# Kernel optimization log

Hardware: AMD Instinct MI355X
Metric: run time of the kernel (lower is better)

Reference implementation:

```python
import jax, jax.numpy as jnp
import numpy as np

T, B, E, H = 1024, 4, 1024, 16
D = E // H  # head_dim = 64


def rel_shift(x):
    # Transformer-XL relative shift trick (RelativeShift.forward, batch_first=True).
    # x: [BH, Q, P] -> pad one zero column, reshape [BH, P+1, Q], drop first row, reshape back.
    BH, Q, P = x.shape
    zp = jnp.zeros((BH, Q, 1), x.dtype)
    xp = jnp.concatenate([zp, x], axis=2).reshape(BH, P + 1, Q)
    return xp[:, 1:, :].reshape(BH, Q, P)


def setup_inputs() -> dict:
    key = jax.random.key(0)
    ks = jax.random.split(key, 8)
    std = float(np.sqrt(2.0 / (E + E)))
    causal = jnp.triu(jnp.ones((T, T), dtype=bool), k=1)  # True = masked (future positions)
    return {
        "x": jax.random.normal(ks[0], (T, B, E), dtype=jnp.float32),
        "pos": jax.random.normal(ks[1], (T, 1, E), dtype=jnp.float32),
        "in_proj_weight": jax.random.normal(ks[2], (3 * E, E), dtype=jnp.float32) * std,
        "in_proj_bias": jnp.zeros((3 * E,), dtype=jnp.float32),
        "out_proj_weight": jax.random.normal(ks[3], (E, E), dtype=jnp.float32) * std,
        "out_proj_bias": jnp.zeros((E,), dtype=jnp.float32),
        "pos_proj_weight": jax.random.normal(ks[4], (E, E), dtype=jnp.float32) * std,
        "pos_proj_bias": jnp.zeros((E,), dtype=jnp.float32),
        "r_w_bias": jax.random.normal(ks[5], (H, D), dtype=jnp.float32) * 0.02,
        "r_r_bias": jax.random.normal(ks[6], (H, D), dtype=jnp.float32) * 0.02,
        "attn_mask": causal,
    }


def reference(x, pos, in_proj_weight, in_proj_bias, out_proj_weight, out_proj_bias,
              pos_proj_weight, pos_proj_bias, r_w_bias, r_r_bias, attn_mask):
    Tq, Bb, Ee = x.shape
    scale = 1.0 / np.sqrt(D).astype(np.float32)
    # fused QKV projection; layout [T, B, heads, 3, head_dim] matches
    # view(len_q, bsz*heads, 3, head_dim) in the original.
    qkv = (x @ in_proj_weight.T + in_proj_bias).reshape(Tq, Bb, H, 3, D)
    q = qkv[..., 0, :]  # [T,B,H,D]
    k = qkv[..., 1, :]
    v = qkv[..., 2, :]
    # position projection (shared across batch since pos is [T,1,E])
    r_head_k = (pos[:, 0, :] @ pos_proj_weight.T + pos_proj_bias).reshape(Tq, H, D)  # [P,H,D]
    rw_q = q + r_w_bias  # content bias
    rr_q = q + r_r_bias  # position bias
    ac = jnp.einsum('qbhd,kbhd->bhqk', rw_q, k) * scale            # [B,H,Q,K]
    bd = jnp.einsum('qbhd,phd->bhqp', rr_q, r_head_k) * scale      # [B,H,Q,P]
    bd = rel_shift(bd.reshape(Bb * H, Tq, Tq)).reshape(Bb, H, Tq, Tq)[..., :Tq]
    score = ac + bd
    score = jnp.where(attn_mask[None, None, :, :], -jnp.inf, score)
    attn = jax.nn.softmax(score, axis=-1)                          # [B,H,Q,K]
    ctx = jnp.einsum('bhqk,kbhd->qbhd', attn, v).reshape(Tq, Bb, Ee)
    out = ctx @ out_proj_weight.T + out_proj_bias                  # [T,B,E]
    return out, attn
```

## Files before the change

### kernel.cpp

```cpp
#include <hip/hip_runtime.h>
#include <math.h>

#define TQ 1024
#define BBATCH 4
#define EDIM 1024
#define HHEADS 16
#define DHEAD 64

typedef __bf16 bf16x8 __attribute__((ext_vector_type(8)));
typedef __bf16 bf16x4 __attribute__((ext_vector_type(4)));
typedef float  f32x4  __attribute__((ext_vector_type(4)));

#define LDK 40

template<int MODE>
__global__ __launch_bounds__(256) void gemm_mfma_abt(
    const float* __restrict__ A, const float* __restrict__ B,
    const float* __restrict__ bias, float* __restrict__ C,
    int M, int N, int K)
{
    __shared__ __bf16 As[128 * LDK];
    __shared__ __bf16 Bs[128 * LDK];
    const int tid  = threadIdx.x;
    const int lane = tid & 63;
    const int wid  = tid >> 6;
    const int wr   = wid >> 1, wc = wid & 1;
    const int m0 = blockIdx.y * 128, n0 = blockIdx.x * 128;

    f32x4 acc[4][4] = {};

    const int sm0 = tid >> 2;
    const int sm1 = sm0 + 64;
    const int sk  = (tid & 3) << 3;

    const int fr = lane & 15;
    const int kg = (lane >> 4) << 3;

    for (int k0 = 0; k0 < K; k0 += 32) {
        float4 ra0a = *(const float4*)&A[(size_t)(m0 + sm0) * K + k0 + sk];
        float4 ra0b = *(const float4*)&A[(size_t)(m0 + sm0) * K + k0 + sk + 4];
        float4 ra1a = *(const float4*)&A[(size_t)(m0 + sm1) * K + k0 + sk];
        float4 ra1b = *(const float4*)&A[(size_t)(m0 + sm1) * K + k0 + sk + 4];
        float4 rb0a = *(const float4*)&B[(size_t)(n0 + sm0) * K + k0 + sk];
        float4 rb0b = *(const float4*)&B[(size_t)(n0 + sm0) * K + k0 + sk + 4];
        float4 rb1a = *(const float4*)&B[(size_t)(n0 + sm1) * K + k0 + sk];
        float4 rb1b = *(const float4*)&B[(size_t)(n0 + sm1) * K + k0 + sk + 4];

        __syncthreads();

        bf16x8 w;
        w[0]=(__bf16)ra0a.x; w[1]=(__bf16)ra0a.y; w[2]=(__bf16)ra0a.z; w[3]=(__bf16)ra0a.w;
        w[4]=(__bf16)ra0b.x; w[5]=(__bf16)ra0b.y; w[6]=(__bf16)ra0b.z; w[7]=(__bf16)ra0b.w;
        *(bf16x8*)&As[sm0 * LDK + sk] = w;
        w[0]=(__bf16)ra1a.x; w[1]=(__bf16)ra1a.y; w[2]=(__bf16)ra1a.z; w[3]=(__bf16)ra1a.w;
        w[4]=(__bf16)ra1b.x; w[5]=(__bf16)ra1b.y; w[6]=(__bf16)ra1b.z; w[7]=(__bf16)ra1b.w;
        *(bf16x8*)&As[sm1 * LDK + sk] = w;
        w[0]=(__bf16)rb0a.x; w[1]=(__bf16)rb0a.y; w[2]=(__bf16)rb0a.z; w[3]=(__bf16)rb0a.w;
        w[4]=(__bf16)rb0b.x; w[5]=(__bf16)rb0b.y; w[6]=(__bf16)rb0b.z; w[7]=(__bf16)rb0b.w;
        *(bf16x8*)&Bs[sm0 * LDK + sk] = w;
        w[0]=(__bf16)rb1a.x; w[1]=(__bf16)rb1a.y; w[2]=(__bf16)rb1a.z; w[3]=(__bf16)rb1a.w;
        w[4]=(__bf16)rb1b.x; w[5]=(__bf16)rb1b.y; w[6]=(__bf16)rb1b.z; w[7]=(__bf16)rb1b.w;
        *(bf16x8*)&Bs[sm1 * LDK + sk] = w;

        __syncthreads();

        bf16x8 af[4], bfr[4];
        #pragma unroll
        for (int i = 0; i < 4; ++i) {
            af[i]  = *(const bf16x8*)&As[(wr * 64 + i * 16 + fr) * LDK + kg];
            bfr[i] = *(const bf16x8*)&Bs[(wc * 64 + i * 16 + fr) * LDK + kg];
        }
        #pragma unroll
        for (int mi = 0; mi < 4; ++mi)
        #pragma unroll
        for (int ni = 0; ni < 4; ++ni)
            acc[mi][ni] = __builtin_amdgcn_mfma_f32_16x16x32_bf16(
                af[mi], bfr[ni], acc[mi][ni], 0, 0, 0);
    }

    const int fq = lane >> 4;
    #pragma unroll
    for (int mi = 0; mi < 4; ++mi)
    #pragma unroll
    for (int ni = 0; ni < 4; ++ni) {
        int row = m0 + wr * 64 + mi * 16 + fq * 4;
        int col = n0 + wc * 64 + ni * 16 + fr;
        float bv = bias[col];
        #pragma unroll
        for (int j = 0; j < 4; ++j) {
            float v = acc[mi][ni][j] + bv;
            if (MODE == 0) {
                C[(size_t)(row + j) * N + col] = v;
            } else {
                C[(((size_t)(col >> 6) << 10) + (row + j)) * 64 + (col & 63)] = v;
            }
        }
    }
}

__global__ __launch_bounds__(256) void bias_dots_kernel(
    const float* __restrict__ qkv, const float* __restrict__ Rm,
    const float* __restrict__ rwb, const float* __restrict__ rrb,
    float* __restrict__ cK, float* __restrict__ cR)
{
    int id = blockIdx.x * 256 + threadIdx.x;
    if (id < 65536) {
        int bh = id >> 10, k = id & 1023;
        int b = bh >> 4, h = bh & 15;
        const float* p = &qkv[((size_t)k * 4 + b) * 3072 + h * 192 + 64];
        const float* w = &rwb[h << 6];
        float s = 0.f;
        #pragma unroll
        for (int d = 0; d < 64; d += 4) {
            float4 v = *(const float4*)&p[d];
            s += v.x * w[d] + v.y * w[d + 1] + v.z * w[d + 2] + v.w * w[d + 3];
        }
        cK[id] = s;
    } else if (id < 81920) {
        int id2 = id - 65536;
        int h = id2 >> 10, j = id2 & 1023;
        const float* p = &Rm[(((size_t)h << 10) + j) * 64];
        const float* w = &rrb[h << 6];
        float s = 0.f;
        #pragma unroll
        for (int d = 0; d < 64; d += 4) {
            float4 v = *(const float4*)&p[d];
            s += v.x * w[d] + v.y * w[d + 1] + v.z * w[d + 2] + v.w * w[d + 3];
        }
        cR[id2] = s;
    }
}

#define SLD 72

__global__ __launch_bounds__(256) void score_mfma_kernel(
    const float* __restrict__ qkv, const float* __restrict__ Rm,
    const float* __restrict__ cK, const float* __restrict__ cR,
    float* __restrict__ attn)
{
    int t = blockIdx.x;
    int qt = (int)((sqrtf(8.f * t + 1.f) - 1.f) * 0.5f);
    while ((qt + 1) * (qt + 2) / 2 <= t) ++qt;
    while (qt * (qt + 1) / 2 > t) --qt;
    int kt = t - qt * (qt + 1) / 2;

    const int bh = blockIdx.y;
    const int b = bh >> 4, h = bh & 15;
    const int q0 = qt << 6, k0 = kt << 6;
    const int tid = threadIdx.x, lane = tid & 63, wid = tid >> 6;
    const int fr = lane & 15, fq = lane >> 4, kg = fq << 3;
    const int w16 = wid << 4;
    const int base_j = k0 - q0 + 960;

    __shared__ __bf16 Qs[64 * SLD];
    __shared__ __bf16 Ks[64 * SLD];
    __shared__ __bf16 Rs[64 * SLD];
    __shared__ float  BDs[64][68];

    float4 qreg[4], kreg[4], r0reg[4], r1reg[4];
    #pragma unroll
    for (int s = 0; s < 4; ++s) {
        int idx = (s << 8) + tid;
        int r = idx >> 4, dc = (idx & 15) << 2;
        qreg[s] = *(const float4*)&qkv[((size_t)(q0 + r) * 4 + b) * 3072 + h * 192 + dc];
        kreg[s] = *(const float4*)&qkv[((size_t)(k0 + r) * 4 + b) * 3072 + h * 192 + 64 + dc];
        int j0 = base_j + r;       if (j0 > 1023) j0 = 1023;
        int j1 = base_j + 64 + r;  if (j1 > 1023) j1 = 1023;
        r0reg[s] = *(const float4*)&Rm[(((size_t)h << 10) + j0) * 64 + dc];
        r1reg[s] = *(const float4*)&Rm[(((size_t)h << 10) + j1) * 64 + dc];
    }
    #pragma unroll
    for (int s = 0; s < 4; ++s) {
        int idx = (s << 8) + tid;
        int r = idx >> 4, dc = (idx & 15) << 2;
        bf16x4 w;
        w[0]=(__bf16)qreg[s].x; w[1]=(__bf16)qreg[s].y; w[2]=(__bf16)qreg[s].z; w[3]=(__bf16)qreg[s].w;
        *(bf16x4*)&Qs[r * SLD + dc] = w;
        w[0]=(__bf16)kreg[s].x; w[1]=(__bf16)kreg[s].y; w[2]=(__bf16)kreg[s].z; w[3]=(__bf16)kreg[s].w;
        *(bf16x4*)&Ks[r * SLD + dc] = w;
        w[0]=(__bf16)r0reg[s].x; w[1]=(__bf16)r0reg[s].y; w[2]=(__bf16)r0reg[s].z; w[3]=(__bf16)r0reg[s].w;
        *(bf16x4*)&Rs[r * SLD + dc] = w;
    }
    __syncthreads();

    bf16x8 af0 = *(const bf16x8*)&Qs[(w16 + fr) * SLD + kg];
    bf16x8 af1 = *(const bf16x8*)&Qs[(w16 + fr) * SLD + 32 + kg];

    f32x4 aac[4], abd[4];
    const f32x4 zero4 = {0.f, 0.f, 0.f, 0.f};

    #pragma unroll
    for (int ni = 0; ni < 4; ++ni) {
        bf16x8 b0 = *(const bf16x8*)&Ks[(ni * 16 + fr) * SLD + kg];
        bf16x8 b1 = *(const bf16x8*)&Ks[(ni * 16 + fr) * SLD + 32 + kg];
        aac[ni] = __builtin_amdgcn_mfma_f32_16x16x32_bf16(af0, b0, zero4, 0, 0, 0);
        aac[ni] = __builtin_amdgcn_mfma_f32_16x16x32_bf16(af1, b1, aac[ni], 0, 0, 0);
    }
    #pragma unroll
    for (int ni = 0; ni < 4; ++ni) {
        bf16x8 b0 = *(const bf16x8*)&Rs[(ni * 16 + fr) * SLD + kg];
        bf16x8 b1 = *(const bf16x8*)&Rs[(ni * 16 + fr) * SLD + 32 + kg];
        abd[ni] = __builtin_amdgcn_mfma_f32_16x16x32_bf16(af0, b0, zero4, 0, 0, 0);
        abd[ni] = __builtin_amdgcn_mfma_f32_16x16x32_bf16(af1, b1, abd[ni], 0, 0, 0);
    }
    #pragma unroll
    for (int ni = 0; ni < 4; ++ni)
    #pragma unroll
    for (int j = 0; j < 4; ++j)
        BDs[w16 + fq * 4 + j][ni * 16 + fr] = abd[ni][j];
    asm volatile("s_waitcnt lgkmcnt(0)" ::: "memory");
    #pragma unroll
    for (int ni = 0; ni < 4; ++ni)
    #pragma unroll
    for (int j = 0; j < 4; ++j) {
        int lrow = w16 + fq * 4 + j;
        int widx = (ni * 16 + fr) - lrow + 63;
        if (widx < 64) aac[ni][j] += BDs[lrow][widx];
    }
    __syncthreads();

    #pragma unroll
    for (int s = 0; s < 4; ++s) {
        int idx = (s << 8) + tid;
        int r = idx >> 4, dc = (idx & 15) << 2;
        bf16x4 w;
        w[0]=(__bf16)r1reg[s].x; w[1]=(__bf16)r1reg[s].y; w[2]=(__bf16)r1reg[s].z; w[3]=(__bf16)r1reg[s].w;
        *(bf16x4*)&Rs[r * SLD + dc] = w;
    }
    __syncthreads();

    #pragma unroll
    for (int ni = 0; ni < 4; ++ni) {
        bf16x8 b0 = *(const bf16x8*)&Rs[(ni * 16 + fr) * SLD + kg];
        bf16x8 b1 = *(const bf16x8*)&Rs[(ni * 16 + fr) * SLD + 32 + kg];
        abd[ni] = __builtin_amdgcn_mfma_f32_16x16x32_bf16(af0, b0, zero4, 0, 0, 0);
        abd[ni] = __builtin_amdgcn_mfma_f32_16x16x32_bf16(af1, b1, abd[ni], 0, 0, 0);
    }
    #pragma unroll
    for (int ni = 0; ni < 4; ++ni)
    #pragma unroll
    for (int j = 0; j < 4; ++j)
        BDs[w16 + fq * 4 + j][ni * 16 + fr] = abd[ni][j];
    asm volatile("s_waitcnt lgkmcnt(0)" ::: "memory");
    #pragma unroll
    for (int ni = 0; ni < 4; ++ni)
    #pragma unroll
    for (int j = 0; j < 4; ++j) {
        int lrow = w16 + fq * 4 + j;
        int widx = (ni * 16 + fr) - lrow + 63;
        if (widx >= 64) aac[ni][j] += BDs[lrow][widx - 64];
    }

    #pragma unroll
    for (int ni = 0; ni < 4; ++ni) {
        int lcol = ni * 16 + fr;
        int k = k0 + lcol;
        float ckv = cK[(bh << 10) + k];
        #pragma unroll
        for (int j = 0; j < 4; ++j) {
            int lrow = w16 + fq * 4 + j;
            int q = q0 + lrow;
            int widx = lcol - lrow + 63;
            int jidx = base_j + widx; if (jidx > 1023) jidx = 1023;
            float crv = cR[(h << 10) + jidx];
            float v = 0.125f * (aac[ni][j] + ckv + crv);
            if (kt == qt && lcol > lrow) v = -1e30f;
            attn[((((size_t)bh << 10) + q) << 10) + k] = v;
        }
    }
}

__global__ __launch_bounds__(256) void row_stats_kernel(
    const float* __restrict__ attn, float2* __restrict__ stats)
{
    const int gw = blockIdx.x * 4 + (threadIdx.x >> 6);
    const int bh = gw >> 10, q = gw & 1023;
    const int lane = threadIdx.x & 63;
    const float* row = attn + ((size_t)bh << 20) + ((size_t)q << 10);

    float m = -1e30f, s = 0.f;
    const int nc = (q >> 8) + 1;
    for (int c = 0; c < nc; ++c) {
        int base = (c << 8) + (lane << 2);
        float4 v = *(const float4*)&row[base];
        bool c0 = base + 0 <= q, c1 = base + 1 <= q, c2 = base + 2 <= q, c3 = base + 3 <= q;
        float e0 = c0 ? v.x : -1e30f, e1 = c1 ? v.y : -1e30f;
        float e2 = c2 ? v.z : -1e30f, e3 = c3 ? v.w : -1e30f;
        float tm = fmaxf(fmaxf(e0, e1), fmaxf(e2, e3));
        float mn = fmaxf(m, tm);
        s *= __expf(m - mn);
        if (c0) s += __expf(v.x - mn);
        if (c1) s += __expf(v.y - mn);
        if (c2) s += __expf(v.z - mn);
        if (c3) s += __expf(v.w - mn);
        m = mn;
    }
    #pragma unroll
    for (int off = 1; off < 64; off <<= 1) {
        float mo = __shfl_xor(m, off), so = __shfl_xor(s, off);
        float mn = fmaxf(m, mo);
        s = s * __expf(m - mn) + so * __expf(mo - mn);
        m = mn;
    }
    if (lane == 0) stats[gw] = make_float2(m, 1.0f / s);
}

#define FLD 66

__global__ __launch_bounds__(256) void ctx_norm_kernel(
    const float* __restrict__ qkv, const float2* __restrict__ stats,
    float* __restrict__ attn, float* __restrict__ ctx)
{
    const int qt = 15 - blockIdx.x;
    const int bh = blockIdx.y;
    const int b = bh >> 4, h = bh & 15;
    const int q0 = qt << 6;
    const int tid = threadIdx.x, lane = tid & 63, wid = tid >> 6;
    const int fr = lane & 15, fq = lane >> 4, kg = fq << 3;
    const int w16 = wid << 4;

    __shared__ __bf16 Pl[64 * FLD];
    __shared__ __bf16 Vt[64 * FLD];

    float mrow[4], inv[4];
    #pragma unroll
    for (int j = 0; j < 4; ++j) {
        float2 st = stats[(bh << 10) + q0 + w16 + fq * 4 + j];
        mrow[j] = st.x; inv[j] = st.y;
    }

    f32x4 apv[4] = {};
    for (int kt = 0; kt <= qt; ++kt) {
        const int k0 = kt << 6;
        float4 vreg[4];
        #pragma unroll
        for (int s = 0; s < 4; ++s) {
            int idx = (s << 8) + tid, r = idx >> 4, dc = (idx & 15) << 2;
            vreg[s] = *(const float4*)&qkv[((size_t)(k0 + r) * 4 + b) * 3072 + h * 192 + 128 + dc];
        }
        float praw[4][4];
        #pragma unroll
        for (int ni = 0; ni < 4; ++ni)
        #pragma unroll
        for (int j = 0; j < 4; ++j)
            praw[ni][j] = attn[((size_t)bh << 20) +
                               ((size_t)(q0 + w16 + fq * 4 + j) << 10) + k0 + ni * 16 + fr];
        __syncthreads();
        #pragma unroll
        for (int s = 0; s < 4; ++s) {
            int idx = (s << 8) + tid, r = idx >> 4, dc = (idx & 15) << 2;
            Vt[(dc + 0) * FLD + r] = (__bf16)vreg[s].x;
            Vt[(dc + 1) * FLD + r] = (__bf16)vreg[s].y;
            Vt[(dc + 2) * FLD + r] = (__bf16)vreg[s].z;
            Vt[(dc + 3) * FLD + r] = (__bf16)vreg[s].w;
        }
        #pragma unroll
        for (int ni = 0; ni < 4; ++ni)
        #pragma unroll
        for (int j = 0; j < 4; ++j) {
            float p = __expf(praw[ni][j] - mrow[j]) * inv[j];
            attn[((size_t)bh << 20) +
                 ((size_t)(q0 + w16 + fq * 4 + j) << 10) + k0 + ni * 16 + fr] = p;
            Pl[(w16 + fq * 4 + j) * FLD + ni * 16 + fr] = (__bf16)p;
        }
        __syncthreads();
        bf16x8 pa0 = *(const bf16x8*)&Pl[(w16 + fr) * FLD + kg];
        bf16x8 pa1 = *(const bf16x8*)&Pl[(w16 + fr) * FLD + 32 + kg];
        #pragma unroll
        for (int ni = 0; ni < 4; ++ni) {
            bf16x8 bv0 = *(const bf16x8*)&Vt[(ni * 16 + fr) * FLD + kg];
            bf16x8 bv1 = *(const bf16x8*)&Vt[(ni * 16 + fr) * FLD + 32 + kg];
            apv[ni] = __builtin_amdgcn_mfma_f32_16x16x32_bf16(pa0, bv0, apv[ni], 0, 0, 0);
            apv[ni] = __builtin_amdgcn_mfma_f32_16x16x32_bf16(pa1, bv1, apv[ni], 0, 0, 0);
        }
    }

    for (int kt = qt + 1; kt < 16; ++kt) {
        const int k0 = kt << 6;
        #pragma unroll
        for (int s = 0; s < 4; ++s) {
            int idx = (s << 8) + tid, r = idx >> 4, c4 = (idx & 15) << 2;
            float4 z = {0.f, 0.f, 0.f, 0.f};
            *(float4*)&attn[((size_t)bh << 20) + ((size_t)(q0 + r) << 10) + k0 + c4] = z;
        }
    }
    #pragma unroll
    for (int ni = 0; ni < 4; ++ni)
    #pragma unroll
    for (int j = 0; j < 4; ++j)
        ctx[((size_t)(q0 + w16 + fq * 4 + j) * 4 + b) * 1024 + (h << 6) + ni * 16 + fr]
            = apv[ni][j];
}

extern "C" void kernel_launch(void* const* d_in, const int* in_sizes, int n_in,
                              void* d_out, int out_size, void* d_ws, size_t ws_size,
                              hipStream_t stream)
{
    (void)in_sizes; (void)n_in; (void)out_size; (void)ws_size;
    const float* x     = (const float*)d_in[0];
    const float* pos   = (const float*)d_in[1];
    const float* w_in  = (const float*)d_in[2];
    const float* b_in  = (const float*)d_in[3];
    const float* w_out = (const float*)d_in[4];
    const float* b_out = (const float*)d_in[5];
    const float* w_pos = (const float*)d_in[6];
    const float* b_pos = (const float*)d_in[7];
    const float* rwb   = (const float*)d_in[8];
    const float* rrb   = (const float*)d_in[9];

    float* out  = (float*)d_out;
    float* attn = out + (size_t)TQ * BBATCH * EDIM;

    float* ws  = (float*)d_ws;
    float* qkv = ws;
    float* R   = qkv + (size_t)4096 * 3072;
    float* ctx = R + (size_t)HHEADS * TQ * DHEAD;
    float*  cK    = out;
    float*  cR    = out + 65536;
    float2* stats = (float2*)(out + 81920);

    dim3 blk(256, 1, 1);

    gemm_mfma_abt<0><<<dim3(3072 / 128, 4096 / 128), blk, 0, stream>>>(
        x, w_in, b_in, qkv, 4096, 3072, 1024);
    gemm_mfma_abt<1><<<dim3(1024 / 128, 1024 / 128), blk, 0, stream>>>(
        pos, w_pos, b_pos, R, 1024, 1024, 1024);
    bias_dots_kernel<<<dim3(320), blk, 0, stream>>>(qkv, R, rwb, rrb, cK, cR);
    score_mfma_kernel<<<dim3(136, 64), blk, 0, stream>>>(qkv, R, cK, cR, attn);
    row_stats_kernel<<<dim3(16384), blk, 0, stream>>>(attn, stats);
    ctx_norm_kernel<<<dim3(16, 64), blk, 0, stream>>>(qkv, stats, attn, ctx);
    gemm_mfma_abt<0><<<dim3(1024 / 128, 4096 / 128), blk, 0, stream>>>(
        ctx, w_out, b_out, out, 4096, 1024, 1024);
}
```

Baseline: 371.8 us.

## Fuse per-tile softmax partial stats into score kernel, drop row-stats pass

The score kernel now computes a per-row max and exp-sum for each 64x64 tile and writes these partials to a scratch buffer. A small reduce kernel combines them into the final row stats. This removes the separate row_stats pass that re-read the whole attention matrix from global memory. The score kernel also stages both R tiles into shared memory up front, aliasing BDs over the Q/K area, which saves one sync round. In exchange it adds shuffle reductions and extra exp work per tile, plus a partials buffer that lives in the output region.

```diff
diff --git a/kernel.cpp b/kernel.cpp
--- a/kernel.cpp
+++ b/kernel.cpp
@@ -133,10 +133,10 @@
 
 #define SLD 72
 
-__global__ __launch_bounds__(256) void score_mfma_kernel(
+__global__ __launch_bounds__(256) void score_tile_kernel(
     const float* __restrict__ qkv, const float* __restrict__ Rm,
     const float* __restrict__ cK, const float* __restrict__ cR,
-    float* __restrict__ attn)
+    float* __restrict__ attn, float2* __restrict__ part)
 {
     int t = blockIdx.x;
     int qt = (int)((sqrtf(8.f * t + 1.f) - 1.f) * 0.5f);
@@ -152,10 +152,12 @@
     const int w16 = wid << 4;
     const int base_j = k0 - q0 + 960;
 
-    __shared__ __bf16 Qs[64 * SLD];
-    __shared__ __bf16 Ks[64 * SLD];
-    __shared__ __bf16 Rs[64 * SLD];
-    __shared__ float  BDs[64][68];
+    __shared__ __align__(16) char smem[36864];
+    __bf16* Qs = (__bf16*)smem;
+    __bf16* Ks = (__bf16*)(smem + 9216);
+    __bf16* R0 = (__bf16*)(smem + 18432);
+    __bf16* R1 = (__bf16*)(smem + 27648);
+    float (*BDs)[68] = (float(*)[68])smem;
 
     float4 qreg[4], kreg[4], r0reg[4], r1reg[4];
     #pragma unroll
@@ -179,7 +181,9 @@
         w[0]=(__bf16)kreg[s].x; w[1]=(__bf16)kreg[s].y; w[2]=(__bf16)kreg[s].z; w[3]=(__bf16)kreg[s].w;
         *(bf16x4*)&Ks[r * SLD + dc] = w;
         w[0]=(__bf16)r0reg[s].x; w[1]=(__bf16)r0reg[s].y; w[2]=(__bf16)r0reg[s].z; w[3]=(__bf16)r0reg[s].w;
-        *(bf16x4*)&Rs[r * SLD + dc] = w;
+        *(bf16x4*)&R0[r * SLD + dc] = w;
+        w[0]=(__bf16)r1reg[s].x; w[1]=(__bf16)r1reg[s].y; w[2]=(__bf16)r1reg[s].z; w[3]=(__bf16)r1reg[s].w;
+        *(bf16x4*)&R1[r * SLD + dc] = w;
     }
     __syncthreads();
 
@@ -187,22 +191,25 @@
     bf16x8 af1 = *(const bf16x8*)&Qs[(w16 + fr) * SLD + 32 + kg];
 
     f32x4 aac[4], abd[4];
-    const f32x4 zero4 = {0.f, 0.f, 0.f, 0.f};
+    const f32x4 z4 = {0.f, 0.f, 0.f, 0.f};
 
     #pragma unroll
     for (int ni = 0; ni < 4; ++ni) {
         bf16x8 b0 = *(const bf16x8*)&Ks[(ni * 16 + fr) * SLD + kg];
         bf16x8 b1 = *(const bf16x8*)&Ks[(ni * 16 + fr) * SLD + 32 + kg];
-        aac[ni] = __builtin_amdgcn_mfma_f32_16x16x32_bf16(af0, b0, zero4, 0, 0, 0);
+        aac[ni] = __builtin_amdgcn_mfma_f32_16x16x32_bf16(af0, b0, z4, 0, 0, 0);
         aac[ni] = __builtin_amdgcn_mfma_f32_16x16x32_bf16(af1, b1, aac[ni], 0, 0, 0);
     }
     #pragma unroll
     for (int ni = 0; ni < 4; ++ni) {
-        bf16x8 b0 = *(const bf16x8*)&Rs[(ni * 16 + fr) * SLD + kg];
-        bf16x8 b1 = *(const bf16x8*)&Rs[(ni * 16 + fr) * SLD + 32 + kg];
-        abd[ni] = __builtin_amdgcn_mfma_f32_16x16x32_bf16(af0, b0, zero4, 0, 0, 0);
+        bf16x8 b0 = *(const bf16x8*)&R0[(ni * 16 + fr) * SLD + kg];
+        bf16x8 b1 = *(const bf16x8*)&R0[(ni * 16 + fr) * SLD + 32 + kg];
+        abd[ni] = __builtin_amdgcn_mfma_f32_16x16x32_bf16(af0, b0, z4, 0, 0, 0);
         abd[ni] = __builtin_amdgcn_mfma_f32_16x16x32_bf16(af1, b1, abd[ni], 0, 0, 0);
     }
+
+    __syncthreads();
+
     #pragma unroll
     for (int ni = 0; ni < 4; ++ni)
     #pragma unroll
@@ -217,23 +224,13 @@
         int widx = (ni * 16 + fr) - lrow + 63;
         if (widx < 64) aac[ni][j] += BDs[lrow][widx];
     }
-    __syncthreads();
-
-    #pragma unroll
-    for (int s = 0; s < 4; ++s) {
-        int idx = (s << 8) + tid;
-        int r = idx >> 4, dc = (idx & 15) << 2;
-        bf16x4 w;
-        w[0]=(__bf16)r1reg[s].x; w[1]=(__bf16)r1reg[s].y; w[2]=(__bf16)r1reg[s].z; w[3]=(__bf16)r1reg[s].w;
-        *(bf16x4*)&Rs[r * SLD + dc] = w;
-    }
-    __syncthreads();
+    asm volatile("s_waitcnt lgkmcnt(0)" ::: "memory");
 
     #pragma unroll
     for (int ni = 0; ni < 4; ++ni) {
-        bf16x8 b0 = *(const bf16x8*)&Rs[(ni * 16 + fr) * SLD + kg];
-        bf16x8 b1 = *(const bf16x8*)&Rs[(ni * 16 + fr) * SLD + 32 + kg];
-        abd[ni] = __builtin_amdgcn_mfma_f32_16x16x32_bf16(af0, b0, zero4, 0, 0, 0);
+        bf16x8 b0 = *(const bf16x8*)&R1[(ni * 16 + fr) * SLD + kg];
+        bf16x8 b1 = *(const bf16x8*)&R1[(ni * 16 + fr) * SLD + 32 + kg];
+        abd[ni] = __builtin_amdgcn_mfma_f32_16x16x32_bf16(af0, b0, z4, 0, 0, 0);
         abd[ni] = __builtin_amdgcn_mfma_f32_16x16x32_bf16(af1, b1, abd[ni], 0, 0, 0);
     }
     #pragma unroll
@@ -251,6 +248,7 @@
         if (widx >= 64) aac[ni][j] += BDs[lrow][widx - 64];
     }
 
+    float sc[4][4];
     #pragma unroll
     for (int ni = 0; ni < 4; ++ni) {
         int lcol = ni * 16 + fr;
@@ -265,44 +263,43 @@
             float crv = cR[(h << 10) + jidx];
             float v = 0.125f * (aac[ni][j] + ckv + crv);
             if (kt == qt && lcol > lrow) v = -1e30f;
+            sc[ni][j] = v;
             attn[((((size_t)bh << 10) + q) << 10) + k] = v;
         }
     }
-}
-
-__global__ __launch_bounds__(256) void row_stats_kernel(
-    const float* __restrict__ attn, float2* __restrict__ stats)
-{
-    const int gw = blockIdx.x * 4 + (threadIdx.x >> 6);
-    const int bh = gw >> 10, q = gw & 1023;
-    const int lane = threadIdx.x & 63;
-    const float* row = attn + ((size_t)bh << 20) + ((size_t)q << 10);
-
-    float m = -1e30f, s = 0.f;
-    const int nc = (q >> 8) + 1;
-    for (int c = 0; c < nc; ++c) {
-        int base = (c << 8) + (lane << 2);
-        float4 v = *(const float4*)&row[base];
-        bool c0 = base + 0 <= q, c1 = base + 1 <= q, c2 = base + 2 <= q, c3 = base + 3 <= q;
-        float e0 = c0 ? v.x : -1e30f, e1 = c1 ? v.y : -1e30f;
-        float e2 = c2 ? v.z : -1e30f, e3 = c3 ? v.w : -1e30f;
-        float tm = fmaxf(fmaxf(e0, e1), fmaxf(e2, e3));
-        float mn = fmaxf(m, tm);
-        s *= __expf(m - mn);
-        if (c0) s += __expf(v.x - mn);
-        if (c1) s += __expf(v.y - mn);
-        if (c2) s += __expf(v.z - mn);
-        if (c3) s += __expf(v.w - mn);
-        m = mn;
-    }
-    #pragma unroll
-    for (int off = 1; off < 64; off <<= 1) {
-        float mo = __shfl_xor(m, off), so = __shfl_xor(s, off);
-        float mn = fmaxf(m, mo);
-        s = s * __expf(m - mn) + so * __expf(mo - mn);
-        m = mn;
-    }
-    if (lane == 0) stats[gw] = make_float2(m, 1.0f / s);
+    #pragma unroll
+    for (int j = 0; j < 4; ++j) {
+        float tmax = fmaxf(fmaxf(sc[0][j], sc[1][j]), fmaxf(sc[2][j], sc[3][j]));
+        tmax = fmaxf(tmax, __shfl_xor(tmax, 1));
+        tmax = fmaxf(tmax, __shfl_xor(tmax, 2));
+        tmax = fmaxf(tmax, __shfl_xor(tmax, 4));
+        tmax = fmaxf(tmax, __shfl_xor(tmax, 8));
+        float ps = __expf(sc[0][j] - tmax) + __expf(sc[1][j] - tmax)
+                 + __expf(sc[2][j] - tmax) + __expf(sc[3][j] - tmax);
+        ps += __shfl_xor(ps, 1); ps += __shfl_xor(ps, 2);
+        ps += __shfl_xor(ps, 4); ps += __shfl_xor(ps, 8);
+        if (fr == 0)
+            part[(((size_t)(bh << 10) + q0 + w16 + fq * 4 + j) << 4) + kt]
+                = make_float2(tmax, ps);
+    }
+}
+
+__global__ __launch_bounds__(256) void stats_reduce_kernel(
+    const float2* __restrict__ part, float2* __restrict__ stats)
+{
+    const int row = blockIdx.x * 256 + threadIdx.x;
+    const int q = row & 1023;
+    const int nt = (q >> 6) + 1;
+    float2 pr[16];
+    float m = -1e30f;
+    for (int kt = 0; kt < nt; ++kt) {
+        pr[kt] = part[((size_t)row << 4) + kt];
+        m = fmaxf(m, pr[kt].x);
+    }
+    float s = 0.f;
+    for (int kt = 0; kt < nt; ++kt)
+        s += pr[kt].y * __expf(pr[kt].x - m);
+    stats[row] = make_float2(m, 1.0f / s);
 }
 
 #define FLD 66
@@ -418,6 +415,7 @@
     float*  cK    = out;
     float*  cR    = out + 65536;
     float2* stats = (float2*)(out + 81920);
+    float2* part  = (float2*)(out + 262144);
 
     dim3 blk(256, 1, 1);
 
@@ -426,8 +424,8 @@
     gemm_mfma_abt<1><<<dim3(1024 / 128, 1024 / 128), blk, 0, stream>>>(
         pos, w_pos, b_pos, R, 1024, 1024, 1024);
     bias_dots_kernel<<<dim3(320), blk, 0, stream>>>(qkv, R, rwb, rrb, cK, cR);
-    score_mfma_kernel<<<dim3(136, 64), blk, 0, stream>>>(qkv, R, cK, cR, attn);
-    row_stats_kernel<<<dim3(16384), blk, 0, stream>>>(attn, stats);
+    score_tile_kernel<<<dim3(136, 64), blk, 0, stream>>>(qkv, R, cK, cR, attn, part);
+    stats_reduce_kernel<<<dim3(256), blk, 0, stream>>>(part, stats);
     ctx_norm_kernel<<<dim3(16, 64), blk, 0, stream>>>(qkv, stats, attn, ctx);
     gemm_mfma_abt<0><<<dim3(1024 / 128, 4096 / 128), blk, 0, stream>>>(
         ctx, w_out, b_out, out, 4096, 1024, 1024);
```

Result: slower. 379.7 us (+2.1%).
